# Optimization experiments

Measured on AMD Instinct MI355X. Metric: run time of the kernel, lower is better.

Reference implementation:

```python
import jax, jax.numpy as jnp
import numpy as np

EPS = 1e-7        # keras backend epsilon
ALPHA = 0.25
GAMMA = 2.0
NEG_INF = -1e30

B, T, V, L = 256, 1024, 128, 64
BLANK = V - 1     # blank_index=-1 in tf ctc_loss_v2


def setup_inputs() -> dict:
    key = jax.random.key(0)
    k1, k2 = jax.random.split(key)
    y_pred = jax.random.uniform(k1, (B, T, V), dtype=jnp.float32)
    y_true = jax.random.randint(k2, (B, L), 0, V - 1, dtype=jnp.int32)
    return {"y_true": y_true, "y_pred": y_pred}


def _ctc_neg_log_lik(y_true, y_pred):
    """Standard CTC forward (alpha) DP in log space; full lengths T and L."""
    b, t, v = y_pred.shape
    l = y_true.shape[1]
    s = 2 * l + 1
    # tf ctc_loss_v2 log-softmaxes its logits; logits here are log(y_pred+eps)
    logp = jax.nn.log_softmax(jnp.log(y_pred + EPS), axis=-1)     # [B,T,V]
    # extended label sequence: blank, l1, blank, l2, ..., blank    [B,S]
    ext = jnp.full((b, s), BLANK, dtype=y_true.dtype)
    ext = ext.at[:, 1::2].set(y_true)
    # per-timestep log-probs of extended labels -> [T,B,S]
    lp_ext = jnp.take_along_axis(logp, ext[:, None, :], axis=2)   # [B,T,S]
    lp_ext = jnp.transpose(lp_ext, (1, 0, 2))                     # [T,B,S]
    # skip transition s-2 -> s allowed iff ext[s] != blank and ext[s] != ext[s-2]
    ext_sm2 = jnp.pad(ext[:, :-2], ((0, 0), (2, 0)), constant_values=BLANK)
    allow_skip = (ext != BLANK) & (ext != ext_sm2)                # [B,S]

    alpha0 = jnp.full((b, s), NEG_INF, dtype=logp.dtype)
    alpha0 = alpha0.at[:, 0].set(lp_ext[0, :, 0])
    alpha0 = alpha0.at[:, 1].set(lp_ext[0, :, 1])

    def step(alpha, lp_t):
        a0 = alpha
        a1 = jnp.pad(alpha[:, :-1], ((0, 0), (1, 0)), constant_values=NEG_INF)
        a2 = jnp.pad(alpha[:, :-2], ((0, 0), (2, 0)), constant_values=NEG_INF)
        a2 = jnp.where(allow_skip, a2, NEG_INF)
        m = jnp.maximum(jnp.maximum(a0, a1), a2)                  # stable LSE
        lse = m + jnp.log(jnp.exp(a0 - m) + jnp.exp(a1 - m) + jnp.exp(a2 - m))
        return lse + lp_t, None

    alphaT, _ = jax.lax.scan(step, alpha0, lp_ext[1:])
    log_lik = jnp.logaddexp(alphaT[:, -1], alphaT[:, -2])         # [B]
    return -log_lik


def reference(y_true, y_pred):
    loss = _ctc_neg_log_lik(y_true, y_pred)                       # [B]
    p = jnp.exp(-loss)
    focal = ALPHA * (1.0 - p) ** GAMMA * loss
    return jnp.mean(focal)
```

## Files before the change

kernel.cpp:

```cpp
#include <hip/hip_runtime.h>


#define EPSF 1e-7f

constexpr int Bb  = 256;
constexpr int Tt  = 1024;
constexpr int Vv  = 128;
constexpr int Ll  = 64;
constexpr int CH  = 128;
constexpr int NCH = Tt / CH;
constexpr int PAIRS = CH / 2;

template <int Ctrl, int RowMask, int BankMask, bool BoundCtrl>
__device__ __forceinline__ float dppf(float x) {
    return __int_as_float(__builtin_amdgcn_update_dpp(
        0, __float_as_int(x), Ctrl, RowMask, BankMask, BoundCtrl));
}

__device__ __forceinline__ float wave_sum63(float x) {
    x += dppf<0x111, 0xf, 0xf, true>(x);
    x += dppf<0x112, 0xf, 0xf, true>(x);
    x += dppf<0x114, 0xf, 0xf, true>(x);
    x += dppf<0x118, 0xf, 0xf, true>(x);
    x += dppf<0x142, 0xa, 0xf, false>(x);
    x += dppf<0x143, 0xc, 0xf, false>(x);
    return x;
}

__device__ __forceinline__ float half_sum(float x) {
    x += dppf<0x111, 0xf, 0xf, true>(x);
    x += dppf<0x112, 0xf, 0xf, true>(x);
    x += dppf<0x114, 0xf, 0xf, true>(x);
    x += dppf<0x118, 0xf, 0xf, true>(x);
    x += dppf<0x142, 0xa, 0xf, false>(x);
    return x;
}

__device__ __forceinline__ float wave_max63(float x) {
    x = fmaxf(x, dppf<0x111, 0xf, 0xf, true>(x));
    x = fmaxf(x, dppf<0x112, 0xf, 0xf, true>(x));
    x = fmaxf(x, dppf<0x114, 0xf, 0xf, true>(x));
    x = fmaxf(x, dppf<0x118, 0xf, 0xf, true>(x));
    x = fmaxf(x, dppf<0x142, 0xa, 0xf, false>(x));
    x = fmaxf(x, dppf<0x143, 0xc, 0xf, false>(x));
    return x;
}

__device__ __forceinline__ float bcast63(float x) {
    return __int_as_float(__builtin_amdgcn_readlane(__float_as_int(x), 63));
}

__launch_bounds__(1024, 1)
__global__ void fused_kernel(const int* __restrict__ y_true,
                             const float* __restrict__ y_pred,
                             float* __restrict__ focal_ws) {
    const int b    = blockIdx.x;
    const int lane = threadIdx.x & 63;
    const int wv   = threadIdx.x >> 6;

    const float*  yb  = y_pred + (size_t)b * Tt * Vv;
    const float4* yb4 = (const float4*)yb;

    __shared__ float4 l4buf[2 * CH * (Vv / 4)];
    __shared__ float  lblk[2 * CH];
    __shared__ float  part[30];
    float* lrows = (float*)l4buf;

    float a_even = 0.0f, a_odd = 0.0f, a128 = 0.0f;
    int   eacc = 0;
    float maskf = 0.0f;
    int   lab = 0;

    const int w    = wv - 1;
    const int half = lane >> 5;
    float ll = 0.0f;

    if (wv == 0) {
        lab = y_true[b * Ll + lane];
        const int labp = __shfl_up(lab, 1);
        maskf  = (lane == 0 || lab != labp) ? 1.0f : 0.0f;
        a_even = (lane == 0) ? 1.0f : 0.0f;
    }

    auto step = [&](float g, float qbl, bool check) {
        const float qe  = g + EPSF;
        const float qb  = qbl + EPSF;
        const float am1 = dppf<0x138, 0xf, 0xf, true>(a_odd);
        const float ne   = (a_even + am1) * qb;
        const float no   = (a_odd + a_even + maskf * am1) * qe;
        const float n128 = (a128 + a_odd) * qb;
        a_even = ne;
        a_odd  = no;
        a128   = n128;
        if (check) {
            const float m = fmaxf(fmaxf(a_even, a_odd), a128);
            if (__all(m < 0x1p-25f)) {
                float mm = wave_max63(m);
                const float    wmax  = bcast63(mm);
                const unsigned e     = __float_as_uint(wmax) >> 23;
                const float    scale = __uint_as_float((254u - e) << 23);
                eacc += (int)e - 127;
                a_even *= scale;
                a_odd  *= scale;
                a128   *= scale;
            }
        }
    };

    for (int p = 0; p <= NCH; ++p) {
        if (wv != 0) {
            if (p < NCH) {
                const int bsel  = p & 1;
                const int gbase = p * CH * (Vv / 4);
                const int lbase = bsel * CH * (Vv / 4);
                float4 v[5];
                int    rpc[5];
#pragma unroll
                for (int k = 0; k < 5; ++k) {
                    const int rp = w + 15 * k;
                    rpc[k] = rp < PAIRS ? rp : PAIRS - 1;
                    v[k]   = yb4[gbase + rpc[k] * 64 + lane];
                }
#pragma unroll
                for (int k = 0; k < 5; ++k) {
                    const bool valid = (w + 15 * k) < PAIRS;
                    if (valid) {
                        l4buf[lbase + rpc[k] * 64 + lane] = v[k];
                        const float s =
                            half_sum(v[k].x + v[k].y + v[k].z + v[k].w);
                        if ((lane & 31) == 31) {
                            lblk[bsel * CH + 2 * rpc[k] + half] = v[k].w;
                            ll += __log2f(s + (float)Vv * EPSF);
                        }
                    }
                }
            } else if ((lane & 31) == 31) {
                part[2 * w + half] = ll;
            }
        } else if (p > 0) {
            const int bsel = (p - 1) & 1;
            const int cb   = bsel * CH * Vv;
            const int bb   = bsel * CH;
            constexpr int PD = 8;
            float gq[PD], bq[PD];
#pragma unroll
            for (int d = 0; d < PD; ++d) {
                gq[d] = lrows[cb + d * Vv + lab];
                bq[d] = lblk[bb + d];
            }
            for (int t0 = 0; t0 < CH - PD; t0 += PD) {
#pragma unroll
                for (int j = 0; j < PD; ++j) {
                    const float g = gq[j];
                    const float q = bq[j];
                    const int  tn = t0 + j + PD;
                    gq[j] = lrows[cb + tn * Vv + lab];
                    bq[j] = lblk[bb + tn];
                    step(g, q, (j & 3) == 3);
                }
            }
#pragma unroll
            for (int j = 0; j < PD; ++j) step(gq[j], bq[j], (j & 3) == 3);
        }
        __syncthreads();
    }

    if (wv == 0) {
        float vs = (lane < 30) ? part[lane] : 0.0f;
        vs = wave_sum63(vs);
        if (lane == 63) {
            const float acc_ld = vs;
            const float tot    = fmaxf(a128 + a_odd, 1e-37f);
            const float log2lik = __log2f(tot) + (float)eacc - acc_ld;
            const float ln_lik  = 0.69314718055994530942f * log2lik;
            const float loss    = -ln_lik;
            const float pp      = __expf(ln_lik);
            const float om      = 1.0f - pp;
            focal_ws[b] = 0.25f * om * om * loss;
        }
    }
}

__global__ void finalize_kernel(const float* __restrict__ focal_ws,
                                float* __restrict__ out) {
    const int i    = threadIdx.x;
    const int lane = i & 63;
    const int wv   = i >> 6;

    float f = focal_ws[i];
#pragma unroll
    for (int off = 32; off > 0; off >>= 1) f += __shfl_xor(f, off);

    __shared__ float red[4];
    if (lane == 0) red[wv] = f;
    __syncthreads();
    if (i == 0)
        out[0] = (red[0] + red[1] + red[2] + red[3]) * (1.0f / (float)Bb);
}

extern "C" void kernel_launch(void* const* d_in, const int* in_sizes, int n_in,
                              void* d_out, int out_size, void* d_ws, size_t ws_size,
                              hipStream_t stream) {
    const int*   y_true = (const int*)d_in[0];
    const float* y_pred = (const float*)d_in[1];
    float* focal_ws = (float*)d_ws;

    fused_kernel<<<Bb, 1024, 0, stream>>>(y_true, y_pred, focal_ws);
    finalize_kernel<<<1, 256, 0, stream>>>(focal_ws, (float*)d_out);
}
```

Before: 200.9 us.

## Add three-stage loader/gather/consumer pipeline with register prefetch for CTC recursion

Restructures the fused CTC kernel into a three-stage pipeline. Thirteen loader waves prefetch the next 64-row chunk into registers while storing the current one to LDS. Two gather waves then pre-extract the per-label probabilities into a contiguous lane-indexed array, and the single DP wave consumes it at raised priority with conflict-free LDS reads. The chunk size halves, rescaling is checked less often with a looser threshold, and barriers use a lighter custom wait, which is meant to take the gather and load latency off the serial recursion path. In exchange it adds more barriers, more LDS, and relies on hand-written waitcnt semantics.

Result: slower. 338.4 us (+68.4%).

```diff
diff --git a/kernel.cpp b/kernel.cpp
--- a/kernel.cpp
+++ b/kernel.cpp
@@ -7,9 +7,11 @@
 constexpr int Tt  = 1024;
 constexpr int Vv  = 128;
 constexpr int Ll  = 64;
-constexpr int CH  = 128;
+constexpr int CH  = 64;
 constexpr int NCH = Tt / CH;
-constexpr int PAIRS = CH / 2;
+constexpr int NPH = NCH + 2;
+constexpr int NLW = 13;
+constexpr int RPW = 3;
 
 template <int Ctrl, int RowMask, int BankMask, bool BoundCtrl>
 __device__ __forceinline__ float dppf(float x) {
@@ -50,6 +52,12 @@
     return __int_as_float(__builtin_amdgcn_readlane(__float_as_int(x), 63));
 }
 
+__device__ __forceinline__ void pipe_barrier() {
+    asm volatile("s_waitcnt lgkmcnt(0)" ::: "memory");
+    __builtin_amdgcn_s_barrier();
+    asm volatile("" ::: "memory");
+}
+
 __launch_bounds__(1024, 1)
 __global__ void fused_kernel(const int* __restrict__ y_true,
                              const float* __restrict__ y_pred,
@@ -58,119 +66,143 @@
     const int lane = threadIdx.x & 63;
     const int wv   = threadIdx.x >> 6;
 
-    const float*  yb  = y_pred + (size_t)b * Tt * Vv;
-    const float4* yb4 = (const float4*)yb;
-
-    __shared__ float4 l4buf[2 * CH * (Vv / 4)];
-    __shared__ float  lblk[2 * CH];
-    __shared__ float  part[30];
-    float* lrows = (float*)l4buf;
-
-    float a_even = 0.0f, a_odd = 0.0f, a128 = 0.0f;
-    int   eacc = 0;
-    float maskf = 0.0f;
-    int   lab = 0;
-
-    const int w    = wv - 1;
+    const float4* yb4 = (const float4*)(y_pred + (size_t)b * Tt * Vv);
+
+    __shared__ float4 tile4[2 * CH * (Vv / 4)];
+    __shared__ float  garr[2 * CH * 64];
+    __shared__ float  lblk[4 * CH];
+    __shared__ float  part[2 * NLW];
+    const float* lrows = (const float*)tile4;
+
+    float a_even = 0.0f, a_odd = 0.0f, a128 = 0.0f, maskf = 0.0f;
+    int   eacc = 0, lab = 0;
+
+    if (wv <= 2) {
+        lab = y_true[b * Ll + lane];
+        if (wv == 0) {
+            const int labp = __shfl_up(lab, 1);
+            maskf  = (lane == 0 || lab != labp) ? 1.0f : 0.0f;
+            a_even = (lane == 0) ? 1.0f : 0.0f;
+        }
+    }
+
+    const int w    = wv - 3;
     const int half = lane >> 5;
+    const int hw   = 2 * w + half;
+    const int c32  = lane & 31;
     float ll = 0.0f;
 
-    if (wv == 0) {
-        lab = y_true[b * Ll + lane];
-        const int labp = __shfl_up(lab, 1);
-        maskf  = (lane == 0 || lab != labp) ? 1.0f : 0.0f;
-        a_even = (lane == 0) ? 1.0f : 0.0f;
-    }
-
-    auto step = [&](float g, float qbl, bool check) {
-        const float qe  = g + EPSF;
-        const float qb  = qbl + EPSF;
-        const float am1 = dppf<0x138, 0xf, 0xf, true>(a_odd);
+    float4 va[RPW], vb[RPW];
+
+    if (wv >= 3) {
+#pragma unroll
+        for (int k = 0; k < RPW; ++k) {
+            const int r = hw + 2 * NLW * k;
+            if (r < CH) va[k] = yb4[r * 32 + c32];
+        }
+    }
+
+    auto do_step = [&](float qe, float qb, bool chk) {
+        const float am1  = dppf<0x138, 0xf, 0xf, true>(a_odd);
         const float ne   = (a_even + am1) * qb;
-        const float no   = (a_odd + a_even + maskf * am1) * qe;
+        const float no   = fmaf(maskf, am1, a_odd + a_even) * qe;
         const float n128 = (a128 + a_odd) * qb;
-        a_even = ne;
-        a_odd  = no;
-        a128   = n128;
-        if (check) {
+        a_even = ne; a_odd = no; a128 = n128;
+        if (chk) {
             const float m = fmaxf(fmaxf(a_even, a_odd), a128);
-            if (__all(m < 0x1p-25f)) {
-                float mm = wave_max63(m);
-                const float    wmax  = bcast63(mm);
+            if (__all(m < 0x1p-75f)) {
+                const float    wmax  = bcast63(wave_max63(m));
                 const unsigned e     = __float_as_uint(wmax) >> 23;
                 const float    scale = __uint_as_float((254u - e) << 23);
                 eacc += (int)e - 127;
-                a_even *= scale;
-                a_odd  *= scale;
-                a128   *= scale;
-            }
-        }
-    };
-
-    for (int p = 0; p <= NCH; ++p) {
-        if (wv != 0) {
-            if (p < NCH) {
-                const int bsel  = p & 1;
-                const int gbase = p * CH * (Vv / 4);
-                const int lbase = bsel * CH * (Vv / 4);
-                float4 v[5];
-                int    rpc[5];
-#pragma unroll
-                for (int k = 0; k < 5; ++k) {
-                    const int rp = w + 15 * k;
-                    rpc[k] = rp < PAIRS ? rp : PAIRS - 1;
-                    v[k]   = yb4[gbase + rpc[k] * 64 + lane];
-                }
-#pragma unroll
-                for (int k = 0; k < 5; ++k) {
-                    const bool valid = (w + 15 * k) < PAIRS;
-                    if (valid) {
-                        l4buf[lbase + rpc[k] * 64 + lane] = v[k];
-                        const float s =
-                            half_sum(v[k].x + v[k].y + v[k].z + v[k].w);
-                        if ((lane & 31) == 31) {
-                            lblk[bsel * CH + 2 * rpc[k] + half] = v[k].w;
-                            ll += __log2f(s + (float)Vv * EPSF);
-                        }
+                a_even *= scale; a_odd *= scale; a128 *= scale;
+            }
+        }
+    };
+
+    auto loader_phase = [&](int p, float4* cur, float4* nxt) {
+        if (p + 1 < NCH) {
+            const int gbase = (p + 1) * CH * (Vv / 4);
+#pragma unroll
+            for (int k = 0; k < RPW; ++k) {
+                const int r = hw + 2 * NLW * k;
+                if (r < CH) nxt[k] = yb4[gbase + r * 32 + c32];
+            }
+        }
+        if (p < NCH) {
+            const int lb4 = (p & 1) * CH * (Vv / 4);
+#pragma unroll
+            for (int k = 0; k < RPW; ++k) {
+                const int r = hw + 2 * NLW * k;
+                if (r < CH) {
+                    tile4[lb4 + r * 32 + c32] = cur[k];
+                    const float s =
+                        half_sum(cur[k].x + cur[k].y + cur[k].z + cur[k].w);
+                    if (c32 == 31) {
+                        lblk[(p & 3) * CH + r] = cur[k].w + EPSF;
+                        ll += __log2f(s + (float)Vv * EPSF);
                     }
                 }
-            } else if ((lane & 31) == 31) {
-                part[2 * w + half] = ll;
-            }
-        } else if (p > 0) {
-            const int bsel = (p - 1) & 1;
-            const int cb   = bsel * CH * Vv;
-            const int bb   = bsel * CH;
-            constexpr int PD = 8;
-            float gq[PD], bq[PD];
-#pragma unroll
-            for (int d = 0; d < PD; ++d) {
-                gq[d] = lrows[cb + d * Vv + lab];
-                bq[d] = lblk[bb + d];
-            }
-            for (int t0 = 0; t0 < CH - PD; t0 += PD) {
-#pragma unroll
-                for (int j = 0; j < PD; ++j) {
-                    const float g = gq[j];
-                    const float q = bq[j];
-                    const int  tn = t0 + j + PD;
-                    gq[j] = lrows[cb + tn * Vv + lab];
-                    bq[j] = lblk[bb + tn];
-                    step(g, q, (j & 3) == 3);
-                }
-            }
-#pragma unroll
-            for (int j = 0; j < PD; ++j) step(gq[j], bq[j], (j & 3) == 3);
-        }
-        __syncthreads();
+            }
+        } else if (p == NCH) {
+            if (c32 == 31) part[hw] = ll;
+        }
+    };
+
+    auto gather_phase = [&](int p) {
+        const int c = p - 1;
+        if (c < 0 || c >= NCH) return;
+        const int sb = (c & 1) * CH * Vv;
+        const int db = (c & 1) * CH * 64;
+        const int t0 = (wv - 1) * 32;
+#pragma unroll 8
+        for (int t = t0; t < t0 + 32; ++t)
+            garr[db + t * 64 + lane] = lrows[sb + t * 128 + lab] + EPSF;
+    };
+
+    auto consumer_phase = [&](int p) {
+        const int c = p - 2;
+        if (c < 0) return;
+        __builtin_amdgcn_s_setprio(1);
+        const float* g  = garr + (c & 1) * CH * 64;
+        const float* bl = lblk + (c & 3) * CH;
+        constexpr int PD = 8;
+        float gq[PD], bq[PD];
+#pragma unroll
+        for (int d = 0; d < PD; ++d) { gq[d] = g[d * 64 + lane]; bq[d] = bl[d]; }
+        for (int t0 = 0; t0 < CH - PD; t0 += PD) {
+            const bool c8 = (t0 & 8) != 0;
+#pragma unroll
+            for (int j = 0; j < PD; ++j) {
+                const float qe = gq[j], qb = bq[j];
+                const int   tn = t0 + j + PD;
+                gq[j] = g[tn * 64 + lane];
+                bq[j] = bl[tn];
+                do_step(qe, qb, c8 && (j == 7));
+            }
+        }
+#pragma unroll
+        for (int j = 0; j < PD; ++j) do_step(gq[j], bq[j], j == 7);
+        __builtin_amdgcn_s_setprio(0);
+    };
+
+    for (int p = 0; p < NPH; p += 2) {
+        if (wv >= 3)      loader_phase(p, va, vb);
+        else if (wv >= 1) gather_phase(p);
+        else              consumer_phase(p);
+        pipe_barrier();
+        if (wv >= 3)      loader_phase(p + 1, vb, va);
+        else if (wv >= 1) gather_phase(p + 1);
+        else              consumer_phase(p + 1);
+        pipe_barrier();
     }
 
     if (wv == 0) {
-        float vs = (lane < 30) ? part[lane] : 0.0f;
+        float vs = (lane < 2 * NLW) ? part[lane] : 0.0f;
         vs = wave_sum63(vs);
         if (lane == 63) {
-            const float acc_ld = vs;
-            const float tot    = fmaxf(a128 + a_odd, 1e-37f);
+            const float acc_ld  = vs;
+            const float tot     = fmaxf(a128 + a_odd, 1e-37f);
             const float log2lik = __log2f(tot) + (float)eacc - acc_ld;
             const float ln_lik  = 0.69314718055994530942f * log2lik;
             const float loss    = -ln_lik;
```

## Decouple DP wave from LDS staging; read labels directly from global

Applied to the files above, without the earlier changes.

Removes the shared-memory double-buffered chunk pipeline and the per-chunk block barriers. Wave 0 now runs the full alpha recursion, prefetching 16 timesteps of label and blank probabilities straight from global memory, with raised priority and a rescale check every 16 steps at a lower threshold. The other waves independently compute the row-sum log normaliser and meet wave 0 at a single barrier. This aims to take the barrier stalls off the serial DP critical path, at the cost of global-memory latency on the dependent gathers and a looser underflow margin.

Measured after the change: 228.0 us. +13.5%, slower.

```diff
diff --git a/kernel.cpp b/kernel.cpp
--- a/kernel.cpp
+++ b/kernel.cpp
@@ -3,13 +3,10 @@
 
 #define EPSF 1e-7f
 
-constexpr int Bb  = 256;
-constexpr int Tt  = 1024;
-constexpr int Vv  = 128;
-constexpr int Ll  = 64;
-constexpr int CH  = 128;
-constexpr int NCH = Tt / CH;
-constexpr int PAIRS = CH / 2;
+constexpr int Bb = 256;
+constexpr int Tt = 1024;
+constexpr int Vv = 128;
+constexpr int Ll = 64;
 
 template <int Ctrl, int RowMask, int BankMask, bool BoundCtrl>
 __device__ __forceinline__ float dppf(float x) {
@@ -50,6 +47,34 @@
     return __int_as_float(__builtin_amdgcn_readlane(__float_as_int(x), 63));
 }
 
+#define DO_STEP(QE, QB, CHK)                                                 \
+    do {                                                                     \
+        const float am1_ = dppf<0x138, 0xf, 0xf, true>(a_odd);               \
+        const float ne_  = (a_even + am1_) * (QB);                           \
+        const float no_  = fmaf(maskf, am1_, a_odd + a_even) * (QE);         \
+        const float n1_  = (a128 + a_odd) * (QB);                            \
+        a_even = ne_; a_odd = no_; a128 = n1_;                               \
+        if (CHK) {                                                           \
+            const float m_ = fmaxf(fmaxf(a_even, a_odd), a128);              \
+            if (__all(m_ < 0x1p-75f)) {                                      \
+                const float    wmax_  = bcast63(wave_max63(m_));             \
+                const unsigned e_     = __float_as_uint(wmax_) >> 23;        \
+                const float    scale_ = __uint_as_float((254u - e_) << 23);  \
+                eacc += (int)e_ - 127;                                       \
+                a_even *= scale_; a_odd *= scale_; a128 *= scale_;           \
+            }                                                                \
+        }                                                                    \
+    } while (0)
+
+#define CSTEP(J, GQ, BQ, CHK)                                                \
+    do {                                                                     \
+        const float qe_ = GQ + EPSF, qb_ = BQ + EPSF;                        \
+        const int   tn_ = t0 + 16 + (J);                                     \
+        GQ = ygl[tn_ * Vv + lab];                                            \
+        BQ = ygl[tn_ * Vv + (Vv - 1)];                                       \
+        DO_STEP(qe_, qb_, CHK);                                              \
+    } while (0)
+
 __launch_bounds__(1024, 1)
 __global__ void fused_kernel(const int* __restrict__ y_true,
                              const float* __restrict__ y_pred,
@@ -58,119 +83,94 @@
     const int lane = threadIdx.x & 63;
     const int wv   = threadIdx.x >> 6;
 
-    const float*  yb  = y_pred + (size_t)b * Tt * Vv;
-    const float4* yb4 = (const float4*)yb;
-
-    __shared__ float4 l4buf[2 * CH * (Vv / 4)];
-    __shared__ float  lblk[2 * CH];
-    __shared__ float  part[30];
-    float* lrows = (float*)l4buf;
-
-    float a_even = 0.0f, a_odd = 0.0f, a128 = 0.0f;
-    int   eacc = 0;
-    float maskf = 0.0f;
-    int   lab = 0;
-
-    const int w    = wv - 1;
-    const int half = lane >> 5;
-    float ll = 0.0f;
-
-    if (wv == 0) {
-        lab = y_true[b * Ll + lane];
+    const float*  ygl = y_pred + (size_t)b * Tt * Vv;
+    const float4* yb4 = (const float4*)ygl;
+
+    __shared__ float part[30];
+
+    if (wv >= 1) {
+        const int hw2 = 2 * (wv - 1) + (lane >> 5);
+        const int c32 = lane & 31;
+        float ll = 0.0f;
+#pragma unroll 5
+        for (int k = 0; k < 35; ++k) {
+            const int r  = hw2 + 30 * k;
+            const int rc = (r < Tt) ? r : (Tt - 1);
+            const float4 v = yb4[rc * (Vv / 4) + c32];
+            const float  s = half_sum(v.x + v.y + v.z + v.w);
+            if (r < Tt && c32 == 31)
+                ll += __log2f(s + (float)Vv * EPSF);
+        }
+        if (c32 == 31) part[hw2] = ll;
+    } else {
+        const int lab = y_true[b * Ll + lane];
         const int labp = __shfl_up(lab, 1);
-        maskf  = (lane == 0 || lab != labp) ? 1.0f : 0.0f;
-        a_even = (lane == 0) ? 1.0f : 0.0f;
-    }
-
-    auto step = [&](float g, float qbl, bool check) {
-        const float qe  = g + EPSF;
-        const float qb  = qbl + EPSF;
-        const float am1 = dppf<0x138, 0xf, 0xf, true>(a_odd);
-        const float ne   = (a_even + am1) * qb;
-        const float no   = (a_odd + a_even + maskf * am1) * qe;
-        const float n128 = (a128 + a_odd) * qb;
-        a_even = ne;
-        a_odd  = no;
-        a128   = n128;
-        if (check) {
-            const float m = fmaxf(fmaxf(a_even, a_odd), a128);
-            if (__all(m < 0x1p-25f)) {
-                float mm = wave_max63(m);
-                const float    wmax  = bcast63(mm);
-                const unsigned e     = __float_as_uint(wmax) >> 23;
-                const float    scale = __uint_as_float((254u - e) << 23);
-                eacc += (int)e - 127;
-                a_even *= scale;
-                a_odd  *= scale;
-                a128   *= scale;
-            }
+        const float maskf = (lane == 0 || lab != labp) ? 1.0f : 0.0f;
+        float a_even = (lane == 0) ? 1.0f : 0.0f;
+        float a_odd = 0.0f, a128 = 0.0f;
+        int   eacc = 0;
+
+        __builtin_amdgcn_s_setprio(1);
+        float gq0  = ygl[0 * Vv + lab],  bq0  = ygl[0 * Vv + Vv - 1];
+        float gq1  = ygl[1 * Vv + lab],  bq1  = ygl[1 * Vv + Vv - 1];
+        float gq2  = ygl[2 * Vv + lab],  bq2  = ygl[2 * Vv + Vv - 1];
+        float gq3  = ygl[3 * Vv + lab],  bq3  = ygl[3 * Vv + Vv - 1];
+        float gq4  = ygl[4 * Vv + lab],  bq4  = ygl[4 * Vv + Vv - 1];
+        float gq5  = ygl[5 * Vv + lab],  bq5  = ygl[5 * Vv + Vv - 1];
+        float gq6  = ygl[6 * Vv + lab],  bq6  = ygl[6 * Vv + Vv - 1];
+        float gq7  = ygl[7 * Vv + lab],  bq7  = ygl[7 * Vv + Vv - 1];
+        float gq8  = ygl[8 * Vv + lab],  bq8  = ygl[8 * Vv + Vv - 1];
+        float gq9  = ygl[9 * Vv + lab],  bq9  = ygl[9 * Vv + Vv - 1];
+        float gq10 = ygl[10 * Vv + lab], bq10 = ygl[10 * Vv + Vv - 1];
+        float gq11 = ygl[11 * Vv + lab], bq11 = ygl[11 * Vv + Vv - 1];
+        float gq12 = ygl[12 * Vv + lab], bq12 = ygl[12 * Vv + Vv - 1];
+        float gq13 = ygl[13 * Vv + lab], bq13 = ygl[13 * Vv + Vv - 1];
+        float gq14 = ygl[14 * Vv + lab], bq14 = ygl[14 * Vv + Vv - 1];
+        float gq15 = ygl[15 * Vv + lab], bq15 = ygl[15 * Vv + Vv - 1];
+
+        for (int t0 = 0; t0 < Tt - 16; t0 += 16) {
+            CSTEP(0,  gq0,  bq0,  false);
+            CSTEP(1,  gq1,  bq1,  false);
+            CSTEP(2,  gq2,  bq2,  false);
+            CSTEP(3,  gq3,  bq3,  false);
+            CSTEP(4,  gq4,  bq4,  false);
+            CSTEP(5,  gq5,  bq5,  false);
+            CSTEP(6,  gq6,  bq6,  false);
+            CSTEP(7,  gq7,  bq7,  false);
+            CSTEP(8,  gq8,  bq8,  false);
+            CSTEP(9,  gq9,  bq9,  false);
+            CSTEP(10, gq10, bq10, false);
+            CSTEP(11, gq11, bq11, false);
+            CSTEP(12, gq12, bq12, false);
+            CSTEP(13, gq13, bq13, false);
+            CSTEP(14, gq14, bq14, false);
+            CSTEP(15, gq15, bq15, true);
         }
-    };
-
-    for (int p = 0; p <= NCH; ++p) {
-        if (wv != 0) {
-            if (p < NCH) {
-                const int bsel  = p & 1;
-                const int gbase = p * CH * (Vv / 4);
-                const int lbase = bsel * CH * (Vv / 4);
-                float4 v[5];
-                int    rpc[5];
-#pragma unroll
-                for (int k = 0; k < 5; ++k) {
-                    const int rp = w + 15 * k;
-                    rpc[k] = rp < PAIRS ? rp : PAIRS - 1;
-                    v[k]   = yb4[gbase + rpc[k] * 64 + lane];
-                }
-#pragma unroll
-                for (int k = 0; k < 5; ++k) {
-                    const bool valid = (w + 15 * k) < PAIRS;
-                    if (valid) {
-                        l4buf[lbase + rpc[k] * 64 + lane] = v[k];
-                        const float s =
-                            half_sum(v[k].x + v[k].y + v[k].z + v[k].w);
-                        if ((lane & 31) == 31) {
-                            lblk[bsel * CH + 2 * rpc[k] + half] = v[k].w;
-                            ll += __log2f(s + (float)Vv * EPSF);
-                        }
-                    }
-                }
-            } else if ((lane & 31) == 31) {
-                part[2 * w + half] = ll;
-            }
-        } else if (p > 0) {
-            const int bsel = (p - 1) & 1;
-            const int cb   = bsel * CH * Vv;
-            const int bb   = bsel * CH;
-            constexpr int PD = 8;
-            float gq[PD], bq[PD];
-#pragma unroll
-            for (int d = 0; d < PD; ++d) {
-                gq[d] = lrows[cb + d * Vv + lab];
-                bq[d] = lblk[bb + d];
-            }
-            for (int t0 = 0; t0 < CH - PD; t0 += PD) {
-#pragma unroll
-                for (int j = 0; j < PD; ++j) {
-                    const float g = gq[j];
-                    const float q = bq[j];
-                    const int  tn = t0 + j + PD;
-                    gq[j] = lrows[cb + tn * Vv + lab];
-                    bq[j] = lblk[bb + tn];
-                    step(g, q, (j & 3) == 3);
-                }
-            }
-#pragma unroll
-            for (int j = 0; j < PD; ++j) step(gq[j], bq[j], (j & 3) == 3);
-        }
+        DO_STEP(gq0 + EPSF,  bq0 + EPSF,  false);
+        DO_STEP(gq1 + EPSF,  bq1 + EPSF,  false);
+        DO_STEP(gq2 + EPSF,  bq2 + EPSF,  false);
+        DO_STEP(gq3 + EPSF,  bq3 + EPSF,  false);
+        DO_STEP(gq4 + EPSF,  bq4 + EPSF,  false);
+        DO_STEP(gq5 + EPSF,  bq5 + EPSF,  false);
+        DO_STEP(gq6 + EPSF,  bq6 + EPSF,  false);
+        DO_STEP(gq7 + EPSF,  bq7 + EPSF,  false);
+        DO_STEP(gq8 + EPSF,  bq8 + EPSF,  false);
+        DO_STEP(gq9 + EPSF,  bq9 + EPSF,  false);
+        DO_STEP(gq10 + EPSF, bq10 + EPSF, false);
+        DO_STEP(gq11 + EPSF, bq11 + EPSF, false);
+        DO_STEP(gq12 + EPSF, bq12 + EPSF, false);
+        DO_STEP(gq13 + EPSF, bq13 + EPSF, false);
+        DO_STEP(gq14 + EPSF, bq14 + EPSF, false);
+        DO_STEP(gq15 + EPSF, bq15 + EPSF, true);
+        __builtin_amdgcn_s_setprio(0);
+
         __syncthreads();
-    }
-
-    if (wv == 0) {
+
         float vs = (lane < 30) ? part[lane] : 0.0f;
         vs = wave_sum63(vs);
         if (lane == 63) {
-            const float acc_ld = vs;
-            const float tot    = fmaxf(a128 + a_odd, 1e-37f);
+            const float acc_ld  = vs;
+            const float tot     = fmaxf(a128 + a_odd, 1e-37f);
             const float log2lik = __log2f(tot) + (float)eacc - acc_ld;
             const float ln_lik  = 0.69314718055994530942f * log2lik;
             const float loss    = -ln_lik;
@@ -178,7 +178,9 @@
             const float om      = 1.0f - pp;
             focal_ws[b] = 0.25f * om * om * loss;
         }
+        return;
     }
+    __syncthreads();
 }
 
 __global__ void finalize_kernel(const float* __restrict__ focal_ws,
```
